# Performance work log

Measured on AMD Instinct MI355X. Metric: run time of the kernel, lower is better.

## Reference

```python
import jax, jax.numpy as jnp
import numpy as np

N = 100000   # nodes
DEG = 32     # in-degree per node
E = N * DEG  # 3.2M edges
D = 24       # node feature dim
NK = 2       # number of anisotropic kernels (tile(...,2) in source forces 2)
H = 64       # MLP hidden/out channels


def setup_inputs() -> dict:
    key = jax.random.key(0)
    k1, k2, k3, k4 = jax.random.split(key, 4)
    x = jax.random.normal(k1, (N, D), dtype=jnp.float32)
    src = jax.random.randint(k2, (E,), 0, N)
    tgt = jnp.repeat(jnp.arange(N), DEG)  # every node has DEG in-edges -> no 0/0
    edge_index = jnp.stack([src, tgt]).astype(jnp.int64)
    kvals = jax.random.normal(k3, (NK, E), dtype=jnp.float32)
    # Linear(2*D -> H, bias=False), xavier-like scale
    W = jax.random.normal(k4, (H, NK * D), dtype=jnp.float32) * (1.0 / (NK * D))
    return {"x": x, "edge_index": edge_index, "kvals": kvals, "W": W}


def reference(x, edge_index, kvals, W):
    src, tgt = edge_index[0], edge_index[1]
    xs = x[src]  # [E, D] gathered source features
    # per-kernel sparse aggregation: out_k[i] = sum_{e: tgt[e]==i} kvals[k,e] * x[src[e]]
    out = jnp.concatenate(
        [jax.ops.segment_sum(kvals[k][:, None] * xs, tgt, num_segments=N)
         for k in range(NK)], axis=1)  # [N, NK*D]
    # adj_norm: subtract tiled neighbor mean
    deg = jax.ops.segment_sum(jnp.ones((E,), x.dtype), tgt, num_segments=N)  # [N]
    sum_x = jax.ops.segment_sum(xs, tgt, num_segments=N)  # [N, D]
    norm_x = sum_x / deg[:, None]
    out = out - jnp.tile(norm_x, (1, NK)) + jnp.tile(x, (1, NK))
    # MLP: single bias-free linear, no activation
    return out @ W.T  # [N, H]
```

## Files before the change

### kernel.cpp

```cpp
#include <hip/hip_runtime.h>


#define NN   100000
#define DEG  32
#define EE   (NN * DEG)
#define DD   24
#define HH   64
#define NPB  32
#define TPB  256
#define NPW  8
#define PST  56

typedef __attribute__((ext_vector_type(8)))  short short8;
typedef __attribute__((ext_vector_type(16))) float float16;

__device__ __forceinline__ unsigned short f2bf(float f) {
    union { float f; unsigned u; } v; v.f = f;
    unsigned r = v.u + 0x7fffu + ((v.u >> 16) & 1u);
    return (unsigned short)(r >> 16);
}

__device__ __forceinline__ float bf2f(unsigned u) {
    union { unsigned i; float f; } v; v.i = u << 16; return v.f;
}

__device__ __forceinline__ unsigned pk(unsigned a, unsigned b) {
    return __builtin_amdgcn_perm(b, a, 0x05040100u);
}

__device__ __forceinline__ short8 mk8(unsigned u0, unsigned u1, unsigned u2, unsigned u3) {
    union { unsigned u[4]; short8 s; } p;
    p.u[0] = u0; p.u[1] = u1; p.u[2] = u2; p.u[3] = u3;
    return p.s;
}

__device__ __forceinline__ void gl_lds4(const void* g, void* l) {
    __builtin_amdgcn_global_load_lds(
        (const __attribute__((address_space(1))) void*)g,
        (__attribute__((address_space(3))) void*)l, 4, 0, 0);
}

__global__ void xcvt(const float* __restrict__ x, unsigned short* __restrict__ xb, int n4) {
    int i = blockIdx.x * blockDim.x + threadIdx.x;
    if (i < n4) {
        float4 v = ((const float4*)x)[i];
        ushort4 o;
        o.x = f2bf(v.x); o.y = f2bf(v.y); o.z = f2bf(v.z); o.w = f2bf(v.w);
        ((ushort4*)xb)[i] = o;
    }
}

__global__ __launch_bounds__(TPB, 4) void gnn(
    const unsigned short* __restrict__ xb,
    const int*            __restrict__ ei,
    const float*          __restrict__ kv,
    const float*          __restrict__ W,
    float*                __restrict__ out)
{
    __shared__ int            ei_s[NPB * DEG];
    __shared__ unsigned short kv_s[2 * NPB * DEG];
    __shared__ unsigned short xv_s[NPB * DD];
    __shared__ unsigned short pre_s[NPB * PST];
    __shared__ __align__(16) char tiles[4][2][2048];

    const int t    = threadIdx.x;
    const int lane = t & 63;
    const int w    = t >> 6;
    const int m    = lane & 31;
    const int kh   = lane >> 5;
    const int kh8  = kh * 8;
    const int t4   = lane >> 4;
    const int dsl  = lane & 15;
    const int base = blockIdx.x * NPB;
    const char* xbc = (const char*)xb;

    {
        const size_t eb = (size_t)base * DEG;
        int4 ev = ((const int4*)(ei + eb))[t];
        ev.x *= 48; ev.y *= 48; ev.z *= 48; ev.w *= 48;
        ((int4*)ei_s)[t] = ev;
        const float4 c0 = ((const float4*)(kv + eb))[t];
        const float4 c1 = ((const float4*)(kv + EE + eb))[t];
        ushort4 u0, u1;
        u0.x = f2bf(c0.x); u0.y = f2bf(c0.y); u0.z = f2bf(c0.z); u0.w = f2bf(c0.w);
        u1.x = f2bf(c1.x); u1.y = f2bf(c1.y); u1.z = f2bf(c1.z); u1.w = f2bf(c1.w);
        ((ushort4*)kv_s)[t] = u0;
        ((ushort4*)(kv_s + NPB * DEG))[t] = u1;
        if (t < (NPB * DD) / 4)
            ((ushort4*)xv_s)[t] = ((const ushort4*)(xb + (size_t)base * DD))[t];
    }
    __syncthreads();

    const unsigned short* kvrow = kv_s + (m & 1) * (NPB * DEG);
    const int n0 = w * NPW;

    #define ISSUE(nl) do {                                                     \
        char* tb_ = tiles[w][(nl) & 1];                                        \
        _Pragma("unroll")                                                      \
        for (int i_ = 0; i_ < 8; ++i_) {                                       \
            const int eo_ = ei_s[(nl) * DEG + i_ * 4 + t4];                    \
            const char* gp_ = (dsl < 12) ? (xbc + (unsigned)(eo_ + dsl * 4))   \
                                         : xbc;                                \
            gl_lds4(gp_, tb_ + i_ * 256);                                      \
        }                                                                      \
    } while (0)

    ISSUE(n0);

    #pragma unroll
    for (int p = 0; p < NPW; ++p) {
        const int nl = n0 + p;
        if (p < NPW - 1) {
            ISSUE(nl + 1);
            __builtin_amdgcn_s_waitcnt(0xF78);
        } else {
            __builtin_amdgcn_s_waitcnt(0xF70);
        }

        const unsigned short* tile = (const unsigned short*)tiles[w][p & 1];

        unsigned r0 = tile[(kh8 + 0) * 32 + m], r1 = tile[(kh8 + 1) * 32 + m];
        unsigned r2 = tile[(kh8 + 2) * 32 + m], r3 = tile[(kh8 + 3) * 32 + m];
        unsigned r4 = tile[(kh8 + 4) * 32 + m], r5 = tile[(kh8 + 5) * 32 + m];
        unsigned r6 = tile[(kh8 + 6) * 32 + m], r7 = tile[(kh8 + 7) * 32 + m];
        const short8 bf0 = mk8(pk(r0, r1), pk(r2, r3), pk(r4, r5), pk(r6, r7));
        unsigned s0 = tile[(16 + kh8 + 0) * 32 + m], s1 = tile[(16 + kh8 + 1) * 32 + m];
        unsigned s2 = tile[(16 + kh8 + 2) * 32 + m], s3 = tile[(16 + kh8 + 3) * 32 + m];
        unsigned s4 = tile[(16 + kh8 + 4) * 32 + m], s5 = tile[(16 + kh8 + 5) * 32 + m];
        unsigned s6 = tile[(16 + kh8 + 6) * 32 + m], s7 = tile[(16 + kh8 + 7) * 32 + m];
        const short8 bf1 = mk8(pk(s0, s1), pk(s2, s3), pk(s4, s5), pk(s6, s7));

        const int el = nl * DEG + kh8;
        const short8 raw0 = *(const short8*)(kvrow + el);
        const short8 raw1 = *(const short8*)(kvrow + el + 16);
        const unsigned fill = (m == 2) ? 0x3F803F80u : 0u;
        const short8 af0 = (m < 2) ? raw0 : mk8(fill, fill, fill, fill);
        const short8 af1 = (m < 2) ? raw1 : mk8(fill, fill, fill, fill);

        float16 acc;
        #pragma unroll
        for (int r = 0; r < 16; ++r) acc[r] = 0.f;
        acc = __builtin_amdgcn_mfma_f32_32x32x16_bf16(af0, bf0, acc, 0, 0, 0);
        acc = __builtin_amdgcn_mfma_f32_32x32x16_bf16(af1, bf1, acc, 0, 0, 0);

        if (kh == 0 && m < DD) {
            const float sm = acc[2] * (1.f / 32.f);
            const float pv = bf2f((unsigned)xv_s[nl * DD + m]) - sm;
            pre_s[nl * PST + m]      = f2bf(acc[0] + pv);
            pre_s[nl * PST + 24 + m] = f2bf(acc[1] + pv);
        }
    }
    #undef ISSUE
    __syncthreads();

    if (w < 2) {
        const int h = w * 32 + m;

        float16 acc;
        #pragma unroll
        for (int r = 0; r < 16; ++r) acc[r] = 0.f;

        #pragma unroll
        for (int kc = 0; kc < 3; ++kc) {
            const int c0 = kc * 16 + kh8;
            const short8 af = *(const short8*)(pre_s + m * PST + c0);
            const float* wr = W + h * 48 + c0;
            const float4 wA = ((const float4*)wr)[0];
            const float4 wB = ((const float4*)wr)[1];
            const short8 bf = mk8(pk(f2bf(wA.x), f2bf(wA.y)), pk(f2bf(wA.z), f2bf(wA.w)),
                                  pk(f2bf(wB.x), f2bf(wB.y)), pk(f2bf(wB.z), f2bf(wB.w)));
            acc = __builtin_amdgcn_mfma_f32_32x32x16_bf16(af, bf, acc, 0, 0, 0);
        }

        #pragma unroll
        for (int r = 0; r < 16; ++r) {
            const int row = (r & 3) + 8 * (r >> 2) + 4 * kh;
            out[(size_t)(base + row) * HH + h] = acc[r];
        }
    }
}

extern "C" void kernel_launch(void* const* d_in, const int* in_sizes, int n_in,
                              void* d_out, int out_size, void* d_ws, size_t ws_size,
                              hipStream_t stream) {
    const float* x  = (const float*)d_in[0];
    const int*   ei = (const int*)d_in[1];
    const float* kv = (const float*)d_in[2];
    const float* W  = (const float*)d_in[3];
    float* out = (float*)d_out;

    unsigned short* xb = (unsigned short*)d_ws;
    const int n4 = NN * DD / 4;
    xcvt<<<(n4 + 255) / 256, 256, 0, stream>>>(x, xb, n4);

    const int grid = NN / NPB;
    gnn<<<grid, TPB, 0, stream>>>(xb, ei, kv, W, out);
}
```

Before: 130.1 us.

## Gather neighbor rows with 16-byte global-to-LDS loads, two nodes per stage

```diff
diff --git a/kernel.cpp b/kernel.cpp
--- a/kernel.cpp
+++ b/kernel.cpp
@@ -34,10 +34,10 @@
     return p.s;
 }
 
-__device__ __forceinline__ void gl_lds4(const void* g, void* l) {
+__device__ __forceinline__ void gl_lds16(const void* g, void* l) {
     __builtin_amdgcn_global_load_lds(
         (const __attribute__((address_space(1))) void*)g,
-        (__attribute__((address_space(3))) void*)l, 4, 0, 0);
+        (__attribute__((address_space(3))) void*)l, 16, 0, 0);
 }
 
 __global__ void xcvt(const float* __restrict__ x, unsigned short* __restrict__ xb, int n4) {
@@ -61,7 +61,7 @@
     __shared__ unsigned short kv_s[2 * NPB * DEG];
     __shared__ unsigned short xv_s[NPB * DD];
     __shared__ unsigned short pre_s[NPB * PST];
-    __shared__ __align__(16) char tiles[4][2][2048];
+    __shared__ __align__(16) char tiles[4][2][3072];
 
     const int t    = threadIdx.x;
     const int lane = t & 63;
@@ -69,8 +69,6 @@
     const int m    = lane & 31;
     const int kh   = lane >> 5;
     const int kh8  = kh * 8;
-    const int t4   = lane >> 4;
-    const int dsl  = lane & 15;
     const int base = blockIdx.x * NPB;
     const char* xbc = (const char*)xb;
 
@@ -91,66 +89,81 @@
     }
     __syncthreads();
 
+    int e_[3], co_[3];
+    #pragma unroll
+    for (int i = 0; i < 3; ++i) {
+        const int ci = i * 64 + lane;
+        e_[i]  = ci / 3;
+        co_[i] = (ci % 3) * 16;
+    }
+
     const unsigned short* kvrow = kv_s + (m & 1) * (NPB * DEG);
-    const int n0 = w * NPW;
-
-    #define ISSUE(nl) do {                                                     \
-        char* tb_ = tiles[w][(nl) & 1];                                        \
+    const int p0 = w * 4;
+
+    #define ISSUE(pr, buf) do {                                                \
+        char* tb_ = tiles[w][buf];                                             \
         _Pragma("unroll")                                                      \
-        for (int i_ = 0; i_ < 8; ++i_) {                                       \
-            const int eo_ = ei_s[(nl) * DEG + i_ * 4 + t4];                    \
-            const char* gp_ = (dsl < 12) ? (xbc + (unsigned)(eo_ + dsl * 4))   \
-                                         : xbc;                                \
-            gl_lds4(gp_, tb_ + i_ * 256);                                      \
+        for (int i_ = 0; i_ < 3; ++i_) {                                       \
+            const int off_ = ei_s[(pr) * 64 + e_[i_]];                         \
+            gl_lds16(xbc + (unsigned)(off_ + co_[i_]), tb_ + i_ * 1024);       \
         }                                                                      \
     } while (0)
 
-    ISSUE(n0);
+    #define COMP(nl, buf) do {                                                 \
+        const unsigned short* tile = (const unsigned short*)tiles[w][buf];     \
+        const int lb = ((nl) & 1) * 32;                                        \
+        unsigned r0 = tile[(lb + kh8 + 0) * 24 + m];                           \
+        unsigned r1 = tile[(lb + kh8 + 1) * 24 + m];                           \
+        unsigned r2 = tile[(lb + kh8 + 2) * 24 + m];                           \
+        unsigned r3 = tile[(lb + kh8 + 3) * 24 + m];                           \
+        unsigned r4 = tile[(lb + kh8 + 4) * 24 + m];                           \
+        unsigned r5 = tile[(lb + kh8 + 5) * 24 + m];                           \
+        unsigned r6 = tile[(lb + kh8 + 6) * 24 + m];                           \
+        unsigned r7 = tile[(lb + kh8 + 7) * 24 + m];                           \
+        const short8 bf0 = mk8(pk(r0, r1), pk(r2, r3), pk(r4, r5), pk(r6, r7)); \
+        unsigned s0 = tile[(lb + 16 + kh8 + 0) * 24 + m];                      \
+        unsigned s1 = tile[(lb + 16 + kh8 + 1) * 24 + m];                      \
+        unsigned s2 = tile[(lb + 16 + kh8 + 2) * 24 + m];                      \
+        unsigned s3 = tile[(lb + 16 + kh8 + 3) * 24 + m];                      \
+        unsigned s4 = tile[(lb + 16 + kh8 + 4) * 24 + m];                      \
+        unsigned s5 = tile[(lb + 16 + kh8 + 5) * 24 + m];                      \
+        unsigned s6 = tile[(lb + 16 + kh8 + 6) * 24 + m];                      \
+        unsigned s7 = tile[(lb + 16 + kh8 + 7) * 24 + m];                      \
+        const short8 bf1 = mk8(pk(s0, s1), pk(s2, s3), pk(s4, s5), pk(s6, s7)); \
+        const int el = (nl) * DEG + kh8;                                       \
+        const short8 raw0 = *(const short8*)(kvrow + el);                      \
+        const short8 raw1 = *(const short8*)(kvrow + el + 16);                 \
+        const unsigned fill = (m == 2) ? 0x3F803F80u : 0u;                     \
+        const short8 af0 = (m < 2) ? raw0 : mk8(fill, fill, fill, fill);       \
+        const short8 af1 = (m < 2) ? raw1 : mk8(fill, fill, fill, fill);       \
+        float16 acc;                                                           \
+        _Pragma("unroll")                                                      \
+        for (int r = 0; r < 16; ++r) acc[r] = 0.f;                             \
+        acc = __builtin_amdgcn_mfma_f32_32x32x16_bf16(af0, bf0, acc, 0, 0, 0); \
+        acc = __builtin_amdgcn_mfma_f32_32x32x16_bf16(af1, bf1, acc, 0, 0, 0); \
+        if (kh == 0 && m < DD) {                                               \
+            const float sm = acc[2] * (1.f / 32.f);                            \
+            const float pv = bf2f((unsigned)xv_s[(nl) * DD + m]) - sm;         \
+            pre_s[(nl) * PST + m]      = f2bf(acc[0] + pv);                    \
+            pre_s[(nl) * PST + 24 + m] = f2bf(acc[1] + pv);                    \
+        }                                                                      \
+    } while (0)
+
+    ISSUE(p0, 0);
 
     #pragma unroll
-    for (int p = 0; p < NPW; ++p) {
-        const int nl = n0 + p;
-        if (p < NPW - 1) {
-            ISSUE(nl + 1);
-            __builtin_amdgcn_s_waitcnt(0xF78);
+    for (int p = 0; p < 4; ++p) {
+        if (p < 3) {
+            ISSUE(p0 + p + 1, (p + 1) & 1);
+            __builtin_amdgcn_s_waitcnt(0xF73);
         } else {
             __builtin_amdgcn_s_waitcnt(0xF70);
         }
-
-        const unsigned short* tile = (const unsigned short*)tiles[w][p & 1];
-
-        unsigned r0 = tile[(kh8 + 0) * 32 + m], r1 = tile[(kh8 + 1) * 32 + m];
-        unsigned r2 = tile[(kh8 + 2) * 32 + m], r3 = tile[(kh8 + 3) * 32 + m];
-        unsigned r4 = tile[(kh8 + 4) * 32 + m], r5 = tile[(kh8 + 5) * 32 + m];
-        unsigned r6 = tile[(kh8 + 6) * 32 + m], r7 = tile[(kh8 + 7) * 32 + m];
-        const short8 bf0 = mk8(pk(r0, r1), pk(r2, r3), pk(r4, r5), pk(r6, r7));
-        unsigned s0 = tile[(16 + kh8 + 0) * 32 + m], s1 = tile[(16 + kh8 + 1) * 32 + m];
-        unsigned s2 = tile[(16 + kh8 + 2) * 32 + m], s3 = tile[(16 + kh8 + 3) * 32 + m];
-        unsigned s4 = tile[(16 + kh8 + 4) * 32 + m], s5 = tile[(16 + kh8 + 5) * 32 + m];
-        unsigned s6 = tile[(16 + kh8 + 6) * 32 + m], s7 = tile[(16 + kh8 + 7) * 32 + m];
-        const short8 bf1 = mk8(pk(s0, s1), pk(s2, s3), pk(s4, s5), pk(s6, s7));
-
-        const int el = nl * DEG + kh8;
-        const short8 raw0 = *(const short8*)(kvrow + el);
-        const short8 raw1 = *(const short8*)(kvrow + el + 16);
-        const unsigned fill = (m == 2) ? 0x3F803F80u : 0u;
-        const short8 af0 = (m < 2) ? raw0 : mk8(fill, fill, fill, fill);
-        const short8 af1 = (m < 2) ? raw1 : mk8(fill, fill, fill, fill);
-
-        float16 acc;
-        #pragma unroll
-        for (int r = 0; r < 16; ++r) acc[r] = 0.f;
-        acc = __builtin_amdgcn_mfma_f32_32x32x16_bf16(af0, bf0, acc, 0, 0, 0);
-        acc = __builtin_amdgcn_mfma_f32_32x32x16_bf16(af1, bf1, acc, 0, 0, 0);
-
-        if (kh == 0 && m < DD) {
-            const float sm = acc[2] * (1.f / 32.f);
-            const float pv = bf2f((unsigned)xv_s[nl * DD + m]) - sm;
-            pre_s[nl * PST + m]      = f2bf(acc[0] + pv);
-            pre_s[nl * PST + 24 + m] = f2bf(acc[1] + pv);
-        }
+        COMP(p0 * 2 + 2 * p,     p & 1);
+        COMP(p0 * 2 + 2 * p + 1, p & 1);
     }
     #undef ISSUE
+    #undef COMP
     __syncthreads();
 
     if (w < 2) {
```

Measured after the change: 127.6 us. About the same (-2.0%).
